# Performance work log

Measured on AMD Instinct MI355X. Metric: run time of the kernel, lower is better.

Reference implementation:

```python
import jax, jax.numpy as jnp
import numpy as np

D_MODEL = 1024
N_HEADS = 16
DH = D_MODEL // N_HEADS            # 64
M = int(round(DH * np.log(DH)))    # 266 random features
KERNEL_EPS = 1e-4
NORM_STAB = 1e-6


def _orthogonal_features(rng):
    # Blocks of orthogonal rows (Q^T from QR of gaussian), scaled by sqrt(DH)
    # (regularize_feature_norms=True path of _generate_feature_matrix).
    blocks = []
    n_full = M // DH
    for _ in range(n_full):
        q, _ = np.linalg.qr(rng.standard_normal((DH, DH)).astype(np.float32))
        blocks.append(q.T)
    rem = M - n_full * DH
    if rem > 0:
        q, _ = np.linalg.qr(rng.standard_normal((DH, DH)).astype(np.float32))
        blocks.append(q.T[:rem])
    W = np.concatenate(blocks, axis=0) * np.sqrt(DH)
    return jnp.asarray(W, dtype=jnp.float32)  # [M, DH]


def setup_inputs() -> dict:
    key = jax.random.key(0)
    ks = jax.random.split(key, 12)
    B, L, D = 2, 8192, D_MODEL
    s = 1.0 / np.sqrt(D)
    inp = {
        "query": jax.random.normal(ks[0], (B, L, D), jnp.float32),
        "key":   jax.random.normal(ks[1], (B, L, D), jnp.float32),
        "value": jax.random.normal(ks[2], (B, L, D), jnp.float32),
        "mask":  jnp.ones((B, L), jnp.float32),
        "Wq": jax.random.normal(ks[3], (D, D), jnp.float32) * s,
        "bq": jnp.zeros((D,), jnp.float32),
        "Wk": jax.random.normal(ks[4], (D, D), jnp.float32) * s,
        "bk": jnp.zeros((D,), jnp.float32),
        "Wv": jax.random.normal(ks[5], (D, D), jnp.float32) * s,
        "bv": jnp.zeros((D,), jnp.float32),
        "Wo": jax.random.normal(ks[6], (D, D), jnp.float32) * s,
        "bo": jnp.zeros((D,), jnp.float32),
        "W_feat": _orthogonal_features(np.random.default_rng(0)),  # [M, DH]
    }
    return inp


def reference(query, key, value, mask, Wq, bq, Wk, bk, Wv, bv, Wo, bo, W_feat):
    B, L, D = query.shape

    def split_heads(x):  # [B,L,D] -> [B,H,L,DH]
        return x.reshape(B, L, N_HEADS, DH).transpose(0, 2, 1, 3)

    q = split_heads(query @ Wq.T + bq)
    k = split_heads(key   @ Wk.T + bk)
    v = split_heads(value @ Wv.T + bv)

    # FAVOR+ with 'exp' kernel
    scale = D ** -0.25
    q = q * scale
    k = k * scale
    proj_q = jnp.einsum('bhld,md->bhlm', q, W_feat)
    proj_k = jnp.einsum('bhld,md->bhlm', k, W_feat)

    h_q = -0.5 * jnp.sum(q * q, axis=-1, keepdims=True)  # [B,H,L,1]
    h_k = -0.5 * jnp.sum(k * k, axis=-1, keepdims=True)
    q_stab = h_q                 # gather of argmax over a size-1 axis == itself
    k_stab = jnp.max(h_k)        # global scalar stabilizer

    q_kern = jnp.exp(h_q + (proj_q - q_stab))   # == exp(proj_q)
    k_kern = jnp.exp(h_k + (proj_k - k_stab))
    nc = M ** -0.5
    q_prime = nc * (q_kern + KERNEL_EPS)        # [B,H,L,M]
    k_prime = nc * (k_kern + KERNEL_EPS)

    # key padding mask multiplies k'
    k_prime = k_prime * mask[:, None, :, None]

    # linear attention: q' @ (k'^T @ v), O(L*M*DH)
    kv = jnp.einsum('bhlm,bhld->bhmd', k_prime, v)     # [B,H,M,DH]
    out = jnp.einsum('bhlm,bhmd->bhld', q_prime, kv)   # [B,H,L,DH]

    # normalization denominator with stabilizer
    d = jnp.einsum('bhlm,bhm->bhl', q_prime, jnp.sum(k_prime, axis=2))[..., None]
    d = d + 2.0 * NORM_STAB * (jnp.abs(d) <= NORM_STAB).astype(d.dtype)
    out = out / d

    ctx = out.transpose(0, 2, 1, 3).reshape(B, L, D)
    return ctx @ Wo.T + bo
```

## Files before the change

### kernel.cpp

```cpp
#include <hip/hip_runtime.h>
#include <hip/hip_bf16.h>


using bf16 = __hip_bfloat16;

typedef short s4v __attribute__((ext_vector_type(4)));
typedef short s8v __attribute__((ext_vector_type(8)));
typedef float f4v __attribute__((ext_vector_type(4)));

#define MFMA16(a, b, c) __builtin_amdgcn_mfma_f32_16x16x32_bf16((a), (b), (c), 0, 0, 0)

#define GLD16(gp, lp)                                                      \
  __builtin_amdgcn_global_load_lds(                                        \
      (__attribute__((address_space(1))) void*)(gp),                       \
      (__attribute__((address_space(3))) void*)(lp), 16, 0, 0)

__device__ __forceinline__ float b2f(bf16 x) { return __bfloat162float(x); }
__device__ __forceinline__ bf16 f2b(float x) { return __float2bfloat16(x); }
__device__ __forceinline__ short f2bs(float x) {
  bf16 h = __float2bfloat16(x);
  short s; __builtin_memcpy(&s, &h, 2); return s;
}
__device__ __forceinline__ float braw(short u) {
  unsigned int t = ((unsigned int)(unsigned short)u) << 16;
  float f; __builtin_memcpy(&f, &t, 4); return f;
}
__device__ __forceinline__ float cexp(float x) { return __expf(fminf(x, 30.f)); }
__device__ __forceinline__ f4v f4zero() {
  f4v z; z[0] = 0.f; z[1] = 0.f; z[2] = 0.f; z[3] = 0.f; return z;
}
__device__ __forceinline__ s8v s8zero() {
  s8v z;
#pragma unroll
  for (int i = 0; i < 8; i++) z[i] = 0;
  return z;
}

#define SCALE_QK 0.1767766952966369f
#define NCONST   0.06131393394849658f
#define KEPS     1e-4f

__global__ __launch_bounds__(256)
void convk(const float* __restrict__ s, bf16* __restrict__ d, int n) {
  const int i = (blockIdx.x * 256 + threadIdx.x) * 4;
  if (i + 3 < n) {
    const float4 f = *(const float4*)(s + i);
    s4v p;
    p[0] = f2bs(f.x); p[1] = f2bs(f.y); p[2] = f2bs(f.z); p[3] = f2bs(f.w);
    *(s4v*)(d + i) = p;
  }
}

__global__ __launch_bounds__(256, 2)
void gemm_a32(const float* __restrict__ A, const bf16* __restrict__ W,
              const float* __restrict__ bias, bf16* __restrict__ C,
              float scale) {
  __shared__ __align__(16) bf16 sA[128 * 32];
  __shared__ __align__(16) bf16 sB[128 * 32];
  const int tid = threadIdx.x;
  const int wave = tid >> 6, lane = tid & 63, quad = lane >> 4, l16 = lane & 15;
  const int wm = (wave & 1) * 64, wn = (wave >> 1) * 64;
  const size_t row0 = (size_t)blockIdx.x * 128, col0 = (size_t)blockIdx.y * 128;
  const int ar = tid >> 1, ac = (tid & 1) * 16;
  const float* gA = A + (row0 + ar) * 1024 + ac;
  const int ldr = tid >> 2, ldc8 = (tid & 3) * 8;
  const bf16* gB = W + (col0 + ldr) * 1024 + ldc8;

  f4v acc[4][4];
#pragma unroll
  for (int i = 0; i < 4; i++)
#pragma unroll
    for (int j = 0; j < 4; j++) acc[i][j] = f4zero();

  for (int k0 = 0; k0 < 1024; k0 += 32) {
    GLD16(gB + k0,         &sB[wave * 512]);
    GLD16(gB + 65536 + k0, &sB[2048 + wave * 512]);
    {
      const float4 f0 = *(const float4*)(gA + k0);
      const float4 f1 = *(const float4*)(gA + k0 + 4);
      const float4 f2 = *(const float4*)(gA + k0 + 8);
      const float4 f3 = *(const float4*)(gA + k0 + 12);
      s8v p0, p1;
      p0[0] = f2bs(f0.x); p0[1] = f2bs(f0.y); p0[2] = f2bs(f0.z); p0[3] = f2bs(f0.w);
      p0[4] = f2bs(f1.x); p0[5] = f2bs(f1.y); p0[6] = f2bs(f1.z); p0[7] = f2bs(f1.w);
      p1[0] = f2bs(f2.x); p1[1] = f2bs(f2.y); p1[2] = f2bs(f2.z); p1[3] = f2bs(f2.w);
      p1[4] = f2bs(f3.x); p1[5] = f2bs(f3.y); p1[6] = f2bs(f3.z); p1[7] = f2bs(f3.w);
      *(s8v*)&sA[ar * 32 + ac]     = p0;
      *(s8v*)&sA[ar * 32 + ac + 8] = p1;
    }
    __syncthreads();
    s8v af[4], bfr[4];
#pragma unroll
    for (int i = 0; i < 4; i++)
      af[i] = *(const s8v*)&sA[(wm + i * 16 + l16) * 32 + quad * 8];
#pragma unroll
    for (int j = 0; j < 4; j++)
      bfr[j] = *(const s8v*)&sB[(wn + j * 16 + l16) * 32 + quad * 8];
#pragma unroll
    for (int i = 0; i < 4; i++)
#pragma unroll
      for (int j = 0; j < 4; j++) acc[i][j] = MFMA16(af[i], bfr[j], acc[i][j]);
    __syncthreads();
  }
#pragma unroll
  for (int j = 0; j < 4; j++) {
    const int col = wn + j * 16 + l16;
    const float bv = bias[col0 + col];
#pragma unroll
    for (int i = 0; i < 4; i++) {
      const size_t rbase = row0 + wm + i * 16 + quad * 4;
#pragma unroll
      for (int r = 0; r < 4; r++)
        C[(rbase + r) * 1024 + col0 + col] = f2b((acc[i][j][r] + bv) * scale);
    }
  }
}

__global__ __launch_bounds__(256, 2)
void gemm_a16(const bf16* __restrict__ A, const bf16* __restrict__ W,
              const float* __restrict__ bias, float* __restrict__ C) {
  __shared__ __align__(16) bf16 sA[128 * 32];
  __shared__ __align__(16) bf16 sB[128 * 32];
  const int tid = threadIdx.x;
  const int wave = tid >> 6, lane = tid & 63, quad = lane >> 4, l16 = lane & 15;
  const int wm = (wave & 1) * 64, wn = (wave >> 1) * 64;
  const size_t row0 = (size_t)blockIdx.x * 128, col0 = (size_t)blockIdx.y * 128;
  const int ldr = tid >> 2, ldc8 = (tid & 3) * 8;
  const bf16* gA = A + (row0 + ldr) * 1024 + ldc8;
  const bf16* gB = W + (col0 + ldr) * 1024 + ldc8;

  f4v acc[4][4];
#pragma unroll
  for (int i = 0; i < 4; i++)
#pragma unroll
    for (int j = 0; j < 4; j++) acc[i][j] = f4zero();

  for (int k0 = 0; k0 < 1024; k0 += 32) {
    GLD16(gA + k0,         &sA[wave * 512]);
    GLD16(gA + 65536 + k0, &sA[2048 + wave * 512]);
    GLD16(gB + k0,         &sB[wave * 512]);
    GLD16(gB + 65536 + k0, &sB[2048 + wave * 512]);
    __syncthreads();
    s8v af[4], bfr[4];
#pragma unroll
    for (int i = 0; i < 4; i++)
      af[i] = *(const s8v*)&sA[(wm + i * 16 + l16) * 32 + quad * 8];
#pragma unroll
    for (int j = 0; j < 4; j++)
      bfr[j] = *(const s8v*)&sB[(wn + j * 16 + l16) * 32 + quad * 8];
#pragma unroll
    for (int i = 0; i < 4; i++)
#pragma unroll
      for (int j = 0; j < 4; j++) acc[i][j] = MFMA16(af[i], bfr[j], acc[i][j]);
    __syncthreads();
  }
#pragma unroll
  for (int j = 0; j < 4; j++) {
    const int col = wn + j * 16 + l16;
    const float bv = bias[col0 + col];
#pragma unroll
    for (int i = 0; i < 4; i++) {
      const size_t rbase = row0 + wm + i * 16 + quad * 4;
#pragma unroll
      for (int r = 0; r < 4; r++)
        C[(rbase + r) * 1024 + col0 + col] = acc[i][j][r] + bv;
    }
  }
}

__global__ __launch_bounds__(256)
void hk_max(const bf16* __restrict__ Kmat, float* __restrict__ bmax) {
  const int tid = threadIdx.x;
  const int idx = blockIdx.x * 256 + tid;
  const bf16* p = Kmat + (size_t)(idx >> 4) * 1024 + (idx & 15) * 64;
  float s = 0.f;
#pragma unroll
  for (int i = 0; i < 8; i++) {
    s8v v = *(const s8v*)(p + i * 8);
#pragma unroll
    for (int e = 0; e < 8; e++) { float x = braw(v[e]); s += x * x; }
  }
  float h = -0.5f * s;
#pragma unroll
  for (int off = 32; off > 0; off >>= 1) h = fmaxf(h, __shfl_down(h, off, 64));
  __shared__ float wmax[4];
  if ((tid & 63) == 0) wmax[tid >> 6] = h;
  __syncthreads();
  if (tid == 0)
    bmax[blockIdx.x] = fmaxf(fmaxf(wmax[0], wmax[1]), fmaxf(wmax[2], wmax[3]));
}

__global__ __launch_bounds__(256)
void kred(const float* __restrict__ bmax, float* __restrict__ kstab) {
  const int tid = threadIdx.x;
  float m = -3.0e38f;
  for (int i = tid; i < 1024; i += 256) m = fmaxf(m, bmax[i]);
#pragma unroll
  for (int off = 32; off > 0; off >>= 1) m = fmaxf(m, __shfl_down(m, off, 64));
  __shared__ float wmax[4];
  if ((tid & 63) == 0) wmax[tid >> 6] = m;
  __syncthreads();
  if (tid == 0)
    *kstab = fmaxf(fmaxf(wmax[0], wmax[1]), fmaxf(wmax[2], wmax[3]));
}

__global__ __launch_bounds__(256, 2)
void kv_kernel(const bf16* __restrict__ Kmat, const bf16* __restrict__ Vmat,
               const bf16* __restrict__ Wf, const float* __restrict__ mask,
               const float* __restrict__ kstab, float* __restrict__ kv,
               float* __restrict__ ksum) {
  __shared__ __align__(16) bf16 sK[64 * 64];
  __shared__ __align__(16) bf16 sVt[64 * 88];
  __shared__ __align__(16) bf16 sKp[272 * 88];
  __shared__ float sHp[256];
  __shared__ float sH[64];
  __shared__ float sMask[64];
  __shared__ float sKsum[272];

  const int tid = threadIdx.x;
  const int wave = tid >> 6, lane = tid & 63, quad = lane >> 4, l16 = lane & 15;
  const int ci = blockIdx.x, bh = blockIdx.y;
  const int b = bh >> 4, h = bh & 15;
  const int l0 = ci * 512;
  const float kst = *kstab;

  for (int i = tid; i < 272; i += 256) sKsum[i] = 0.f;

  f4v acc[17];
#pragma unroll
  for (int j = 0; j < 17; j++) acc[j] = f4zero();

  const int vr = tid >> 3, vc8 = (tid & 7) * 8;
  const int hr = tid & 63, hp = tid >> 6;

  for (int sc = 0; sc < 8; sc++) {
    const size_t grow = (size_t)b * 8192 + l0 + sc * 64;
    GLD16(Kmat + (grow + vr) * 1024 + h * 64 + vc8,      &sK[wave * 512]);
    GLD16(Kmat + (grow + 32 + vr) * 1024 + h * 64 + vc8, &sK[2048 + wave * 512]);
#pragma unroll
    for (int i = 0; i < 2; i++) {
      const unsigned short* g =
          (const unsigned short*)(Vmat + (grow + 32 * i + vr) * 1024 + h * 64 + vc8);
      ushort4 a = *(const ushort4*)g;
      ushort4 c = *(const ushort4*)(g + 4);
      const int r = 32 * i + vr;
      unsigned short* sv = (unsigned short*)sVt;
      sv[(vc8 + 0) * 88 + r] = a.x; sv[(vc8 + 1) * 88 + r] = a.y;
      sv[(vc8 + 2) * 88 + r] = a.z; sv[(vc8 + 3) * 88 + r] = a.w;
      sv[(vc8 + 4) * 88 + r] = c.x; sv[(vc8 + 5) * 88 + r] = c.y;
      sv[(vc8 + 6) * 88 + r] = c.z; sv[(vc8 + 7) * 88 + r] = c.w;
    }
    {
      const bf16* g = Kmat + (grow + hr) * 1024 + h * 64 + hp * 16;
      s8v v0 = *(const s8v*)g;
      s8v v1 = *(const s8v*)(g + 8);
      float s = 0.f;
#pragma unroll
      for (int e = 0; e < 8; e++) {
        float x0 = braw(v0[e]); float x1 = braw(v1[e]);
        s += x0 * x0 + x1 * x1;
      }
      sHp[hp * 64 + hr] = s;
      if (hp == 0) sMask[hr] = mask[grow + hr];
    }
    __syncthreads();
    if (tid < 64)
      sH[tid] = -0.5f * (sHp[tid] + sHp[64 + tid] + sHp[128 + tid] + sHp[192 + tid]);
    __syncthreads();
    {
      const s8v aK0 = *(const s8v*)&sK[(wave * 16 + l16) * 64 + quad * 8];
      const s8v aK1 = *(const s8v*)&sK[(wave * 16 + l16) * 64 + 32 + quad * 8];
      const int rb = wave * 16 + quad * 4;
      float hv[4], mv[4];
#pragma unroll
      for (int r = 0; r < 4; r++) { hv[r] = sH[rb + r] - kst; mv[r] = sMask[rb + r]; }
#pragma unroll
      for (int j = 0; j < 17; j++) {
        const int f = j * 16 + l16;
        s8v w0, w1;
        if (f < 266) {
          w0 = *(const s8v*)(Wf + f * 64 + quad * 8);
          w1 = *(const s8v*)(Wf + f * 64 + 32 + quad * 8);
        } else { w0 = s8zero(); w1 = s8zero(); }
        f4v p = f4zero();
        p = MFMA16(aK0, w0, p);
        p = MFMA16(aK1, w1, p);
        if (f < 266) {
          float sk = 0.f;
#pragma unroll
          for (int r = 0; r < 4; r++) {
            float kp = NCONST * (cexp(hv[r] + p[r]) + KEPS) * mv[r];
            sk += kp;
            sKp[f * 88 + rb + r] = f2b(kp);
          }
          atomicAdd(&sKsum[f], sk);
        } else {
#pragma unroll
          for (int r = 0; r < 4; r++) sKp[f * 88 + rb + r] = f2b(0.f);
        }
      }
    }
    __syncthreads();
    {
      const s8v bV0 = *(const s8v*)&sVt[(wave * 16 + l16) * 88 + quad * 8];
      const s8v bV1 = *(const s8v*)&sVt[(wave * 16 + l16) * 88 + 32 + quad * 8];
#pragma unroll
      for (int j = 0; j < 17; j++) {
        const s8v a0 = *(const s8v*)&sKp[(j * 16 + l16) * 88 + quad * 8];
        const s8v a1 = *(const s8v*)&sKp[(j * 16 + l16) * 88 + 32 + quad * 8];
        acc[j] = MFMA16(a0, bV0, acc[j]);
        acc[j] = MFMA16(a1, bV1, acc[j]);
      }
    }
    __syncthreads();
  }
  const int dh = wave * 16 + l16;
#pragma unroll
  for (int j = 0; j < 17; j++) {
    const int fb = j * 16 + quad * 4;
#pragma unroll
    for (int r = 0; r < 4; r++)
      atomicAdd(&kv[((size_t)bh * 272 + fb + r) * 64 + dh], acc[j][r]);
  }
  for (int i = tid; i < 272; i += 256) atomicAdd(&ksum[(size_t)bh * 272 + i], sKsum[i]);
}

__global__ __launch_bounds__(256)
void kvt_kernel(const float* __restrict__ kv, bf16* __restrict__ kvT) {
  const int idx = blockIdx.x * 256 + threadIdx.x;
  const int f = idx % 288;
  const int t2 = idx / 288;
  const int dh = t2 & 63;
  const int bh = t2 >> 6;
  float v = 0.f;
  if (f < 272) v = kv[((size_t)bh * 272 + f) * 64 + dh];
  kvT[idx] = f2b(v);
}

__global__ __launch_bounds__(256, 2)
void out_kernel(const bf16* __restrict__ Qmat, const bf16* __restrict__ Wf,
                const bf16* __restrict__ kvT, const float* __restrict__ ksum,
                bf16* __restrict__ ctx) {
  __shared__ __align__(16) bf16 sQ[64 * 64];
  __shared__ __align__(16) bf16 sQp[64 * 296];
  __shared__ float sKs[272];
  __shared__ float sDp[256];
  __shared__ float sRd[64];

  const int tid = threadIdx.x;
  const int wave = tid >> 6, lane = tid & 63, quad = lane >> 4, l16 = lane & 15;
  const int ci = blockIdx.x, bh = blockIdx.y;
  const int b = bh >> 4, h = bh & 15;
  const size_t grow = (size_t)b * 8192 + ci * 64;

  const int vr = tid >> 3, vc8 = (tid & 7) * 8;
  GLD16(Qmat + (grow + vr) * 1024 + h * 64 + vc8,      &sQ[wave * 512]);
  GLD16(Qmat + (grow + 32 + vr) * 1024 + h * 64 + vc8, &sQ[2048 + wave * 512]);

  for (int i = tid; i < 272; i += 256) sKs[i] = ksum[(size_t)bh * 272 + i];
  {
    const int r = tid >> 2, c = tid & 3;
#pragma unroll
    for (int cc = 0; cc < 4; cc++) sQp[r * 296 + 272 + c * 4 + cc] = f2b(0.f);
  }
  __syncthreads();

  const s8v aQ0 = *(const s8v*)&sQ[(wave * 16 + l16) * 64 + quad * 8];
  const s8v aQ1 = *(const s8v*)&sQ[(wave * 16 + l16) * 64 + 32 + quad * 8];
  const int rb = wave * 16 + quad * 4;
#pragma unroll
  for (int j = 0; j < 17; j++) {
    const int f = j * 16 + l16;
    s8v w0, w1;
    if (f < 266) {
      w0 = *(const s8v*)(Wf + f * 64 + quad * 8);
      w1 = *(const s8v*)(Wf + f * 64 + 32 + quad * 8);
    } else { w0 = s8zero(); w1 = s8zero(); }
    f4v p = f4zero();
    p = MFMA16(aQ0, w0, p);
    p = MFMA16(aQ1, w1, p);
#pragma unroll
    for (int r = 0; r < 4; r++) {
      float qp = (f < 266) ? NCONST * (cexp(p[r]) + KEPS) : 0.f;
      sQp[(rb + r) * 296 + f] = f2b(qp);
    }
  }
  __syncthreads();
  {
    const int r = tid & 63, part = tid >> 6;
    float s = 0.f;
    for (int f = part * 68; f < part * 68 + 68; f++)
      s += b2f(sQp[r * 296 + f]) * sKs[f];
    sDp[part * 64 + r] = s;
  }
  __syncthreads();
  if (tid < 64) {
    float d = sDp[tid] + sDp[64 + tid] + sDp[128 + tid] + sDp[192 + tid];
    if (fabsf(d) <= 1e-6f) d += 2e-6f;
    sRd[tid] = 1.f / d;
  }
  __syncthreads();
  f4v acc[4];
#pragma unroll
  for (int mt = 0; mt < 4; mt++) acc[mt] = f4zero();
  const bf16* kvb = kvT + (size_t)bh * 64 * 288 + (wave * 16 + l16) * 288;
#pragma unroll
  for (int kk = 0; kk < 9; kk++) {
    const s8v bfr = *(const s8v*)(kvb + kk * 32 + quad * 8);
#pragma unroll
    for (int mt = 0; mt < 4; mt++) {
      const s8v a = *(const s8v*)&sQp[(mt * 16 + l16) * 296 + kk * 32 + quad * 8];
      acc[mt] = MFMA16(a, bfr, acc[mt]);
    }
  }
  const int col = wave * 16 + l16;
#pragma unroll
  for (int mt = 0; mt < 4; mt++) {
#pragma unroll
    for (int r = 0; r < 4; r++) {
      const int row = mt * 16 + quad * 4 + r;
      ctx[(grow + row) * 1024 + h * 64 + col] = f2b(acc[mt][r] * sRd[row]);
    }
  }
}

static const size_t OFF_KM    = 0;
static const size_t OFF_CTX   = 0;
static const size_t OFF_WQ    = 33554432;
static const size_t OFF_WK    = OFF_WQ + 2097152;
static const size_t OFF_WV    = OFF_WK + 2097152;
static const size_t OFF_WO    = OFF_WV + 2097152;
static const size_t OFF_WF    = OFF_WO + 2097152;
static const size_t OFF_KV    = OFF_WF + 65536;
static const size_t OFF_KSUM  = OFF_KV + 2228224;
static const size_t OFF_KVT   = OFF_KSUM + 34816;
static const size_t OFF_BMAX  = OFF_KVT + 1179648;
static const size_t OFF_KSTAB = OFF_BMAX + 4096;
static const size_t WS_NEEDED = OFF_KSTAB + 16;

extern "C" void kernel_launch(void* const* d_in, const int* in_sizes, int n_in,
                              void* d_out, int out_size, void* d_ws, size_t ws_size,
                              hipStream_t stream) {
  (void)in_sizes; (void)n_in; (void)out_size;
  if (ws_size < WS_NEEDED) return;
  const float* query = (const float*)d_in[0];
  const float* key_  = (const float*)d_in[1];
  const float* value = (const float*)d_in[2];
  const float* mask  = (const float*)d_in[3];
  const float* Wq = (const float*)d_in[4];
  const float* bq = (const float*)d_in[5];
  const float* Wk = (const float*)d_in[6];
  const float* bk = (const float*)d_in[7];
  const float* Wv = (const float*)d_in[8];
  const float* bv = (const float*)d_in[9];
  const float* Wo = (const float*)d_in[10];
  const float* bo = (const float*)d_in[11];
  const float* Wf = (const float*)d_in[12];

  char* ws = (char*)d_ws;
  bf16*  Qm   = (bf16*)d_out;
  bf16*  Vm   = (bf16*)((char*)d_out + 33554432);
  bf16*  Km   = (bf16*)(ws + OFF_KM);
  bf16*  ctxb = (bf16*)(ws + OFF_CTX);
  bf16*  wqb  = (bf16*)(ws + OFF_WQ);
  bf16*  wkb  = (bf16*)(ws + OFF_WK);
  bf16*  wvb  = (bf16*)(ws + OFF_WV);
  bf16*  wob  = (bf16*)(ws + OFF_WO);
  bf16*  wfb  = (bf16*)(ws + OFF_WF);
  float* kv    = (float*)(ws + OFF_KV);
  float* ksum  = (float*)(ws + OFF_KSUM);
  bf16*  kvT   = (bf16*)(ws + OFF_KVT);
  float* bmax  = (float*)(ws + OFF_BMAX);
  float* kstab = (float*)(ws + OFF_KSTAB);
  float* outp  = (float*)d_out;

  const dim3 blk(256);
  convk<<<dim3(1024), blk, 0, stream>>>(Wq, wqb, 1048576);
  convk<<<dim3(1024), blk, 0, stream>>>(Wk, wkb, 1048576);
  convk<<<dim3(1024), blk, 0, stream>>>(Wv, wvb, 1048576);
  convk<<<dim3(1024), blk, 0, stream>>>(Wo, wob, 1048576);
  convk<<<dim3(17),   blk, 0, stream>>>(Wf, wfb, 17024);

  gemm_a32<<<dim3(128, 8), blk, 0, stream>>>(query, wqb, bq, Qm, SCALE_QK);
  gemm_a32<<<dim3(128, 8), blk, 0, stream>>>(key_,  wkb, bk, Km, SCALE_QK);
  gemm_a32<<<dim3(128, 8), blk, 0, stream>>>(value, wvb, bv, Vm, 1.0f);
  hk_max<<<dim3(1024), blk, 0, stream>>>(Km, bmax);
  kred<<<dim3(1), blk, 0, stream>>>(bmax, kstab);
  hipMemsetAsync(ws + OFF_KV, 0, 2228224 + 34816, stream);
  kv_kernel<<<dim3(16, 32), blk, 0, stream>>>(Km, Vm, wfb, mask, kstab, kv, ksum);
  kvt_kernel<<<dim3(2304), blk, 0, stream>>>(kv, kvT);
  out_kernel<<<dim3(128, 32), blk, 0, stream>>>(Qm, wfb, kvT, ksum, ctxb);
  gemm_a16<<<dim3(128, 8), blk, 0, stream>>>(ctxb, wob, bo, outp);
}
```

Baseline: 689.7 us.

## Restructure kv kernel to per-wave feature tiles and merge weight conversions

The kv kernel is rewritten so each wave owns a fixed set of feature tiles, keeps its W_feat fragments in registers, and processes 32-token chunks with wave-private LDS buffers. This replaces the block-wide __syncthreads barriers and the shared-memory atomics on ksum with wave barriers and shuffle reductions. It also cuts LDS footprint, which may let more blocks run per CU. Separately, the four weight-conversion launches are merged into one 2D-grid kernel to save launch overhead. The work is uneven across waves (wave 0 gets five tiles, the others four), and V is transposed through strided scalar LDS reads.

Result: faster. 627.9 us (-9.0%).

```diff
diff --git a/kernel.cpp b/kernel.cpp
--- a/kernel.cpp
+++ b/kernel.cpp
@@ -39,6 +39,21 @@
 #define SCALE_QK 0.1767766952966369f
 #define NCONST   0.06131393394849658f
 #define KEPS     1e-4f
+
+__global__ __launch_bounds__(256)
+void convw4(const float* __restrict__ s0, const float* __restrict__ s1,
+            const float* __restrict__ s2, const float* __restrict__ s3,
+            bf16* __restrict__ d0, bf16* __restrict__ d1,
+            bf16* __restrict__ d2, bf16* __restrict__ d3) {
+  const int w = blockIdx.y;
+  const float* s = (w == 0) ? s0 : (w == 1) ? s1 : (w == 2) ? s2 : s3;
+  bf16* d = (w == 0) ? d0 : (w == 1) ? d1 : (w == 2) ? d2 : d3;
+  const int i = (blockIdx.x * 256 + threadIdx.x) * 4;
+  const float4 f = *(const float4*)(s + i);
+  s4v p;
+  p[0] = f2bs(f.x); p[1] = f2bs(f.y); p[2] = f2bs(f.z); p[3] = f2bs(f.w);
+  *(s4v*)(d + i) = p;
+}
 
 __global__ __launch_bounds__(256)
 void convk(const float* __restrict__ s, bf16* __restrict__ d, int n) {
@@ -205,124 +220,124 @@
 }
 
 __global__ __launch_bounds__(256, 2)
-void kv_kernel(const bf16* __restrict__ Kmat, const bf16* __restrict__ Vmat,
-               const bf16* __restrict__ Wf, const float* __restrict__ mask,
-               const float* __restrict__ kstab, float* __restrict__ kv,
-               float* __restrict__ ksum) {
-  __shared__ __align__(16) bf16 sK[64 * 64];
-  __shared__ __align__(16) bf16 sVt[64 * 88];
-  __shared__ __align__(16) bf16 sKp[272 * 88];
-  __shared__ float sHp[256];
-  __shared__ float sH[64];
-  __shared__ float sMask[64];
-  __shared__ float sKsum[272];
-
+void kv_kernel2(const bf16* __restrict__ Kmat, const bf16* __restrict__ Vmat,
+                const bf16* __restrict__ Wf, const float* __restrict__ mask,
+                const float* __restrict__ kstab, float* __restrict__ kv,
+                float* __restrict__ ksum) {
+  __shared__ __align__(16) bf16 sV[4][32 * 66];
+  __shared__ __align__(16) bf16 sT[4][5][16 * 40];
   const int tid = threadIdx.x;
   const int wave = tid >> 6, lane = tid & 63, quad = lane >> 4, l16 = lane & 15;
-  const int ci = blockIdx.x, bh = blockIdx.y;
-  const int b = bh >> 4, h = bh & 15;
-  const int l0 = ci * 512;
+  const int bh = blockIdx.y, b = bh >> 4, h = bh & 15;
   const float kst = *kstab;
-
-  for (int i = tid; i < 272; i += 256) sKsum[i] = 0.f;
-
-  f4v acc[17];
-#pragma unroll
-  for (int j = 0; j < 17; j++) acc[j] = f4zero();
-
-  const int vr = tid >> 3, vc8 = (tid & 7) * 8;
-  const int hr = tid & 63, hp = tid >> 6;
-
-  for (int sc = 0; sc < 8; sc++) {
-    const size_t grow = (size_t)b * 8192 + l0 + sc * 64;
-    GLD16(Kmat + (grow + vr) * 1024 + h * 64 + vc8,      &sK[wave * 512]);
-    GLD16(Kmat + (grow + 32 + vr) * 1024 + h * 64 + vc8, &sK[2048 + wave * 512]);
-#pragma unroll
-    for (int i = 0; i < 2; i++) {
-      const unsigned short* g =
-          (const unsigned short*)(Vmat + (grow + 32 * i + vr) * 1024 + h * 64 + vc8);
-      ushort4 a = *(const ushort4*)g;
-      ushort4 c = *(const ushort4*)(g + 4);
-      const int r = 32 * i + vr;
-      unsigned short* sv = (unsigned short*)sVt;
-      sv[(vc8 + 0) * 88 + r] = a.x; sv[(vc8 + 1) * 88 + r] = a.y;
-      sv[(vc8 + 2) * 88 + r] = a.z; sv[(vc8 + 3) * 88 + r] = a.w;
-      sv[(vc8 + 4) * 88 + r] = c.x; sv[(vc8 + 5) * 88 + r] = c.y;
-      sv[(vc8 + 6) * 88 + r] = c.z; sv[(vc8 + 7) * 88 + r] = c.w;
-    }
+  const int NT = (wave == 0) ? 5 : 4;
+
+  s8v wf0[5], wf1[5];
+#pragma unroll
+  for (int t = 0; t < 5; t++) {
+    const int f = (wave + t * 4) * 16 + l16;
+    if (t < NT && f < 266) {
+      wf0[t] = *(const s8v*)(Wf + f * 64 + quad * 8);
+      wf1[t] = *(const s8v*)(Wf + f * 64 + 32 + quad * 8);
+    } else { wf0[t] = s8zero(); wf1[t] = s8zero(); }
+  }
+
+  f4v acc[5][4];
+  float ks[5][4];
+#pragma unroll
+  for (int t = 0; t < 5; t++) {
+#pragma unroll
+    for (int d = 0; d < 4; d++) acc[t][d] = f4zero();
+#pragma unroll
+    for (int r = 0; r < 4; r++) ks[t][r] = 0.f;
+  }
+
+  const size_t base = (size_t)b * 8192 + blockIdx.x * 512;
+  const int svr = lane >> 1, svc = (lane & 1) * 32;
+  bf16* sVb = &sV[wave][0];
+  const unsigned short* sVu = (const unsigned short*)sVb;
+
+  for (int it = 0; it < 16; it++) {
+    const size_t tok0 = base + it * 32;
     {
-      const bf16* g = Kmat + (grow + hr) * 1024 + h * 64 + hp * 16;
-      s8v v0 = *(const s8v*)g;
-      s8v v1 = *(const s8v*)(g + 8);
-      float s = 0.f;
+      const bf16* g = Vmat + (tok0 + svr) * 1024 + h * 64 + svc;
+#pragma unroll
+      for (int c = 0; c < 4; c++)
+        *(s8v*)&sVb[svr * 66 + svc + c * 8] = *(const s8v*)(g + c * 8);
+    }
+#pragma unroll
+    for (int tg = 0; tg < 2; tg++) {
+      const size_t tk = tok0 + tg * 16;
+      const bf16* kp = Kmat + (tk + l16) * 1024 + h * 64;
+      const s8v bk0 = *(const s8v*)(kp + quad * 8);
+      const s8v bk1 = *(const s8v*)(kp + 32 + quad * 8);
+      float ss = 0.f;
 #pragma unroll
       for (int e = 0; e < 8; e++) {
-        float x0 = braw(v0[e]); float x1 = braw(v1[e]);
-        s += x0 * x0 + x1 * x1;
+        float x0 = braw(bk0[e]), x1 = braw(bk1[e]);
+        ss += x0 * x0 + x1 * x1;
       }
-      sHp[hp * 64 + hr] = s;
-      if (hp == 0) sMask[hr] = mask[grow + hr];
-    }
-    __syncthreads();
-    if (tid < 64)
-      sH[tid] = -0.5f * (sHp[tid] + sHp[64 + tid] + sHp[128 + tid] + sHp[192 + tid]);
-    __syncthreads();
-    {
-      const s8v aK0 = *(const s8v*)&sK[(wave * 16 + l16) * 64 + quad * 8];
-      const s8v aK1 = *(const s8v*)&sK[(wave * 16 + l16) * 64 + 32 + quad * 8];
-      const int rb = wave * 16 + quad * 4;
-      float hv[4], mv[4];
-#pragma unroll
-      for (int r = 0; r < 4; r++) { hv[r] = sH[rb + r] - kst; mv[r] = sMask[rb + r]; }
-#pragma unroll
-      for (int j = 0; j < 17; j++) {
-        const int f = j * 16 + l16;
-        s8v w0, w1;
-        if (f < 266) {
-          w0 = *(const s8v*)(Wf + f * 64 + quad * 8);
-          w1 = *(const s8v*)(Wf + f * 64 + 32 + quad * 8);
-        } else { w0 = s8zero(); w1 = s8zero(); }
-        f4v p = f4zero();
-        p = MFMA16(aK0, w0, p);
-        p = MFMA16(aK1, w1, p);
-        if (f < 266) {
-          float sk = 0.f;
+      ss += __shfl_xor(ss, 16, 64);
+      ss += __shfl_xor(ss, 32, 64);
+      const float hh = -0.5f * ss - kst;
+      const float mv = mask[tk + l16];
+#pragma unroll
+      for (int t = 0; t < 5; t++) {
+        if (t < NT) {
+          f4v p = f4zero();
+          p = MFMA16(wf0[t], bk0, p);
+          p = MFMA16(wf1[t], bk1, p);
+          const int fb = (wave + t * 4) * 16 + quad * 4;
+          bf16* buf = &sT[wave][t][0];
 #pragma unroll
           for (int r = 0; r < 4; r++) {
-            float kp = NCONST * (cexp(hv[r] + p[r]) + KEPS) * mv[r];
-            sk += kp;
-            sKp[f * 88 + rb + r] = f2b(kp);
+            const float kp_ = (fb + r < 266)
+                ? NCONST * (cexp(hh + p[r]) + KEPS) * mv : 0.f;
+            ks[t][r] += kp_;
+            buf[(quad * 4 + r) * 40 + tg * 16 + l16] = f2b(kp_);
           }
-          atomicAdd(&sKsum[f], sk);
-        } else {
-#pragma unroll
-          for (int r = 0; r < 4; r++) sKp[f * 88 + rb + r] = f2b(0.f);
         }
       }
     }
-    __syncthreads();
-    {
-      const s8v bV0 = *(const s8v*)&sVt[(wave * 16 + l16) * 88 + quad * 8];
-      const s8v bV1 = *(const s8v*)&sVt[(wave * 16 + l16) * 88 + 32 + quad * 8];
-#pragma unroll
-      for (int j = 0; j < 17; j++) {
-        const s8v a0 = *(const s8v*)&sKp[(j * 16 + l16) * 88 + quad * 8];
-        const s8v a1 = *(const s8v*)&sKp[(j * 16 + l16) * 88 + 32 + quad * 8];
-        acc[j] = MFMA16(a0, bV0, acc[j]);
-        acc[j] = MFMA16(a1, bV1, acc[j]);
+    __builtin_amdgcn_wave_barrier();
+    s8v bv[4];
+#pragma unroll
+    for (int d = 0; d < 4; d++) {
+#pragma unroll
+      for (int j = 0; j < 8; j++)
+        bv[d][j] = (short)sVu[(quad * 8 + j) * 66 + d * 16 + l16];
+    }
+#pragma unroll
+    for (int t = 0; t < 5; t++) {
+      if (t < NT) {
+        const s8v a = *(const s8v*)&sT[wave][t][l16 * 40 + quad * 8];
+#pragma unroll
+        for (int d = 0; d < 4; d++) acc[t][d] = MFMA16(a, bv[d], acc[t][d]);
       }
     }
-    __syncthreads();
-  }
-  const int dh = wave * 16 + l16;
-#pragma unroll
-  for (int j = 0; j < 17; j++) {
-    const int fb = j * 16 + quad * 4;
-#pragma unroll
-    for (int r = 0; r < 4; r++)
-      atomicAdd(&kv[((size_t)bh * 272 + fb + r) * 64 + dh], acc[j][r]);
-  }
-  for (int i = tid; i < 272; i += 256) atomicAdd(&ksum[(size_t)bh * 272 + i], sKsum[i]);
+    __builtin_amdgcn_wave_barrier();
+  }
+#pragma unroll
+  for (int t = 0; t < 5; t++) {
+    if (t < NT) {
+      const int fb = (wave + t * 4) * 16 + quad * 4;
+#pragma unroll
+      for (int r = 0; r < 4; r++) {
+        float s = ks[t][r];
+        s += __shfl_xor(s, 1, 64);
+        s += __shfl_xor(s, 2, 64);
+        s += __shfl_xor(s, 4, 64);
+        s += __shfl_xor(s, 8, 64);
+        if (l16 == 0) atomicAdd(&ksum[(size_t)bh * 272 + fb + r], s);
+      }
+#pragma unroll
+      for (int d = 0; d < 4; d++)
+#pragma unroll
+        for (int r = 0; r < 4; r++)
+          atomicAdd(&kv[((size_t)bh * 272 + fb + r) * 64 + d * 16 + l16],
+                    acc[t][d][r]);
+    }
+  }
 }
 
 __global__ __launch_bounds__(256)
@@ -475,11 +490,8 @@
   float* outp  = (float*)d_out;
 
   const dim3 blk(256);
-  convk<<<dim3(1024), blk, 0, stream>>>(Wq, wqb, 1048576);
-  convk<<<dim3(1024), blk, 0, stream>>>(Wk, wkb, 1048576);
-  convk<<<dim3(1024), blk, 0, stream>>>(Wv, wvb, 1048576);
-  convk<<<dim3(1024), blk, 0, stream>>>(Wo, wob, 1048576);
-  convk<<<dim3(17),   blk, 0, stream>>>(Wf, wfb, 17024);
+  convw4<<<dim3(1024, 4), blk, 0, stream>>>(Wq, Wk, Wv, Wo, wqb, wkb, wvb, wob);
+  convk<<<dim3(17), blk, 0, stream>>>(Wf, wfb, 17024);
 
   gemm_a32<<<dim3(128, 8), blk, 0, stream>>>(query, wqb, bq, Qm, SCALE_QK);
   gemm_a32<<<dim3(128, 8), blk, 0, stream>>>(key_,  wkb, bk, Km, SCALE_QK);
@@ -487,7 +499,7 @@
   hk_max<<<dim3(1024), blk, 0, stream>>>(Km, bmax);
   kred<<<dim3(1), blk, 0, stream>>>(bmax, kstab);
   hipMemsetAsync(ws + OFF_KV, 0, 2228224 + 34816, stream);
-  kv_kernel<<<dim3(16, 32), blk, 0, stream>>>(Km, Vm, wfb, mask, kstab, kv, ksum);
+  kv_kernel2<<<dim3(16, 32), blk, 0, stream>>>(Km, Vm, wfb, mask, kstab, kv, ksum);
   kvt_kernel<<<dim3(2304), blk, 0, stream>>>(kv, kvT);
   out_kernel<<<dim3(128, 32), blk, 0, stream>>>(Qm, wfb, kvT, ksum, ctxb);
   gemm_a16<<<dim3(128, 8), blk, 0, stream>>>(ctxb, wob, bo, outp);
```
